# Kernel optimization log

Measured on AMD Instinct MI355X. Metric: run time of the kernel, lower is better.

## Reference

```python
import jax, jax.numpy as jnp
import numpy as np

SEQ, BATCH, IN, HID, OUT = 4096, 64, 64, 256, 1


def setup_inputs() -> dict:
    key = jax.random.key(0)
    ks = jax.random.split(key, 7)
    s = 1.0 / np.sqrt(HID)  # torch GRU/Linear init scale
    return {
        "x": jax.random.normal(ks[0], (SEQ, BATCH, IN), dtype=jnp.float32),
        "w_ih": jax.random.uniform(ks[1], (3 * HID, IN), jnp.float32, -s, s),
        "w_hh": jax.random.uniform(ks[2], (3 * HID, HID), jnp.float32, -s, s),
        "b_ih": jax.random.uniform(ks[3], (3 * HID,), jnp.float32, -s, s),
        "b_hh": jax.random.uniform(ks[4], (3 * HID,), jnp.float32, -s, s),
        "fc_w": jax.random.uniform(ks[5], (OUT, HID), jnp.float32, -s, s),
        "fc_b": jax.random.uniform(ks[6], (OUT,), jnp.float32, -s, s),
    }


def _gru(x, w_ih, w_hh, b_ih, b_hh):
    # x: [S, B, I]. Precompute input-side gate projections in one big GEMM.
    xg = jnp.einsum("sbi,gi->sbg", x, w_ih) + b_ih  # [S, B, 3H]
    H = w_hh.shape[1]
    h0 = jnp.zeros((x.shape[1], H), x.dtype)

    def step(h, xt):
        hg = h @ w_hh.T + b_hh  # [B, 3H]
        xr, xz, xn = jnp.split(xt, 3, axis=-1)
        hr, hz, hn = jnp.split(hg, 3, axis=-1)
        r = jax.nn.sigmoid(xr + hr)
        z = jax.nn.sigmoid(xz + hz)
        n = jnp.tanh(xn + r * hn)  # torch GRU: r gates the hidden-side n term
        h_new = (1.0 - z) * n + z * h
        return h_new, h_new

    _, hs = jax.lax.scan(step, h0, xg)  # hs: [S, B, H]
    return hs


def reference(x, w_ih, w_hh, b_ih, b_hh, fc_w, fc_b):
    hs = _gru(x, w_ih, w_hh, b_ih, b_hh)  # [S, B, H]
    out = hs @ fc_w.T + fc_b  # [S, B, OUT]
    # original does .squeeze(0): no-op since S != 1
    return out
```

## Files before the change

kernel.cpp:

```cpp
#include <hip/hip_runtime.h>

#define SEQ  4096
#define NB   64
#define NI   64
#define NH   256

typedef short  bf16x8 __attribute__((ext_vector_type(8)));
typedef short  bf16x4 __attribute__((ext_vector_type(4)));
typedef float  f32x4  __attribute__((ext_vector_type(4)));

__device__ __forceinline__ unsigned short f2bf(float f) {
    union { float f; unsigned u; } v; v.f = f;
    return (unsigned short)((v.u + 0x7fffu + ((v.u >> 16) & 1u)) >> 16);
}
__device__ __forceinline__ float bflo(int p) {
    union { int i; float f; } u; u.i = p << 16; return u.f;
}
__device__ __forceinline__ float bfhi(int p) {
    union { int i; float f; } u; u.i = p & 0xffff0000; return u.f;
}
__device__ __forceinline__ float fast_rcp(float x) { return __builtin_amdgcn_rcpf(x); }
__device__ __forceinline__ float sigm(float x) { return fast_rcp(1.f + __expf(-x)); }
__device__ __forceinline__ float tanh_(float x) {
    x = fminf(15.f, fmaxf(-15.f, x));
    float e = __expf(2.f * x);
    return (e - 1.f) * fast_rcp(e + 1.f);
}
__device__ __forceinline__ f32x4 mfma16(bf16x8 a, bf16x8 b, f32x4 c) {
    return __builtin_amdgcn_mfma_f32_16x16x32_bf16(a, b, c, 0, 0, 0);
}
__device__ __forceinline__ bf16x8 ldfrag(const float* p) {
    float4 a = *(const float4*)p;
    float4 b = *(const float4*)(p + 4);
    bf16x8 r;
    r[0] = (short)f2bf(a.x); r[1] = (short)f2bf(a.y);
    r[2] = (short)f2bf(a.z); r[3] = (short)f2bf(a.w);
    r[4] = (short)f2bf(b.x); r[5] = (short)f2bf(b.y);
    r[6] = (short)f2bf(b.z); r[7] = (short)f2bf(b.w);
    return r;
}

__global__ __launch_bounds__(1024) void xg_pre(
        const float* __restrict__ x, const float* __restrict__ w_ih,
        const float* __restrict__ b_ih, const float* __restrict__ b_hh,
        short* __restrict__ xg, size_t plane, int t0, int ns)
{
    const int tid = threadIdx.x, wv = tid >> 6, lane = tid & 63;
    const int nn = lane & 15, q = lane >> 4;
    const int jb = wv;

    bf16x8 w[3][2];
    float bias[3];
    #pragma unroll
    for (int g = 0; g < 3; ++g) {
        const int row = g * NH + jb * 16 + nn;
        w[g][0] = ldfrag(w_ih + row * NI + q * 8);
        w[g][1] = ldfrag(w_ih + row * NI + 32 + q * 8);
        bias[g] = b_ih[row] + (g < 2 ? b_hh[row] : 0.f);
    }

    const int NT = ns * 4;
    for (int rt = blockIdx.x; rt < NT; rt += gridDim.x) {
        const float* xr = x + ((size_t)t0 * NB + (size_t)rt * 16 + nn) * NI + q * 8;
        bf16x8 a0 = ldfrag(xr);
        bf16x8 a1 = ldfrag(xr + 32);
        #pragma unroll
        for (int g = 0; g < 3; ++g) {
            f32x4 acc = {0.f, 0.f, 0.f, 0.f};
            acc = mfma16(a0, w[g][0], acc);
            acc = mfma16(a1, w[g][1], acc);
            bf16x4 v;
            #pragma unroll
            for (int m = 0; m < 4; ++m) v[m] = (short)f2bf(acc[m] + bias[g]);
            *(bf16x4*)(xg + (size_t)g * plane +
                       (((size_t)rt * 16 + jb) * 64 + lane) * 4) = v;
        }
    }
}

__global__ __launch_bounds__(1024, 4) void gru_rec(
        const short* __restrict__ xg, size_t plane,
        const float* __restrict__ w_hh,
        const float* __restrict__ b_hh,
        const float* __restrict__ fc_w,
        const float* __restrict__ fc_b,
        float* __restrict__ out,
        float* __restrict__ hcar,
        int t0, int ns)
{
    __shared__ short wlds[65536];
    __shared__ short abuf[8192];
    __shared__ short fcwl[4096];
    __shared__ float oring[1024];

    const int tid = threadIdx.x, wv = tid >> 6, lane = tid & 63;
    const int nn = lane & 15, q = lane >> 4;
    const int bc = blockIdx.x, bbase = bc * 16;

    bf16x8 wr[8], wz[8];
    #pragma unroll
    for (int c = 0; c < 8; ++c)
        wr[c] = ldfrag(w_hh + (0 * NH + wv * 16 + nn) * NH + c * 32 + q * 8);
    #pragma unroll
    for (int c = 0; c < 8; ++c)
        wz[c] = ldfrag(w_hh + (1 * NH + wv * 16 + nn) * NH + c * 32 + q * 8);
    #pragma unroll
    for (int c = 0; c < 8; ++c) {
        bf16x8 f = ldfrag(w_hh + (2 * NH + wv * 16 + nn) * NH + c * 32 + q * 8);
        *(bf16x8*)(wlds + (wv * 8 + c) * 512 + lane * 8) = f;
    }
    if (wv < 8) {
        bf16x8 f = 0;
        if (nn == 0) f = ldfrag(fc_w + wv * 32 + q * 8);
        *(bf16x8*)(fcwl + wv * 512 + lane * 8) = f;
    }
    const float bhn = b_hh[2 * NH + wv * 16 + nn];
    const float fcb = fc_b[0];

    f32x4 hp = {0.f, 0.f, 0.f, 0.f};
    if (t0 == 0) {
        ((int4*)abuf)[tid] = make_int4(0, 0, 0, 0);
    } else {
        #pragma unroll
        for (int m = 0; m < 4; ++m)
            hp[m] = hcar[(size_t)(bbase + q * 4 + m) * NH + wv * 16 + nn];
        const int f = tid * 4, b = f >> 8, k0 = f & 255;
        float4 v = *(const float4*)(hcar + (size_t)(bbase + b) * NH + k0);
        bf16x4 s; s[0] = (short)f2bf(v.x); s[1] = (short)f2bf(v.y);
        s[2] = (short)f2bf(v.z); s[3] = (short)f2bf(v.w);
        *(bf16x4*)(abuf + (k0 >> 5) * 512 + (((k0 >> 3) & 3) * 16 + b) * 8 + (k0 & 7)) = s;
    }

    const int j = wv * 16 + nn;
    const int koff = (j >> 5) * 512 + ((j >> 3) & 3) * 128 + (j & 7) + q * 32;
    const short* xgp = xg + ((size_t)(bc * 16 + wv) * 64 + lane) * 4;
    __syncthreads();

    for (int t = 0; t < ns; ++t) {
        const int cur = t & 1, nxt = cur ^ 1;

        int2 gx = *(const int2*)(xgp);
        int2 gz = *(const int2*)(xgp + plane);
        int2 gn = *(const int2*)(xgp + 2 * plane);
        xgp += 16384;

        if ((t & 31) == 1 && t >= 33 && tid < 512) {
            const int s0 = t - 33;
            out[((size_t)(t0 + s0 + (tid >> 4))) * NB + bbase + (tid & 15)] =
                oring[(((s0 >> 5) & 1) << 9) + (tid >> 4) * 16 + (tid & 15)];
        }

        const bool isfc = (t > 0) && (wv == (t & 15));
        f32x4 ar = {0.f,0.f,0.f,0.f}, az = {0.f,0.f,0.f,0.f};
        f32x4 an = {0.f,0.f,0.f,0.f}, afc = {0.f,0.f,0.f,0.f};
        const short* ab = abuf + cur * 4096;
        #pragma unroll
        for (int c = 0; c < 8; ++c) {
            bf16x8 av = *(const bf16x8*)(ab + c * 512 + lane * 8);
            ar = mfma16(av, wr[c], ar);
            az = mfma16(av, wz[c], az);
            bf16x8 wnf = *(const bf16x8*)(wlds + (wv * 8 + c) * 512 + lane * 8);
            an = mfma16(av, wnf, an);
            if (isfc) {
                bf16x8 ff = *(const bf16x8*)(fcwl + c * 512 + lane * 8);
                afc = mfma16(av, ff, afc);
            }
        }
        if (isfc && nn == 0) {
            const int s = t - 1;
            f32x4 v;
            #pragma unroll
            for (int m = 0; m < 4; ++m) v[m] = afc[m] + fcb;
            *(f32x4*)(oring + (((s >> 5) & 1) << 9) + ((s & 31) << 4) + q * 4) = v;
        }

        const float xr4[4] = { bflo(gx.x), bfhi(gx.x), bflo(gx.y), bfhi(gx.y) };
        const float xz4[4] = { bflo(gz.x), bfhi(gz.x), bflo(gz.y), bfhi(gz.y) };
        const float xn4[4] = { bflo(gn.x), bfhi(gn.x), bflo(gn.y), bfhi(gn.y) };

        short* hw = abuf + nxt * 4096 + koff;
        #pragma unroll
        for (int m = 0; m < 4; ++m) {
            float r_ = sigm(ar[m] + xr4[m]);
            float z_ = sigm(az[m] + xz4[m]);
            float n_ = tanh_(fmaf(r_, an[m] + bhn, xn4[m]));
            float h_ = n_ + z_ * (hp[m] - n_);
            hp[m] = h_;
            hw[m * 8] = (short)f2bf(h_);
        }
        __syncthreads();
    }

    if (wv == 0) {
        const short* ab = abuf + (ns & 1) * 4096;
        f32x4 afc = {0.f, 0.f, 0.f, 0.f};
        #pragma unroll
        for (int c = 0; c < 8; ++c)
            afc = mfma16(*(const bf16x8*)(ab + c * 512 + lane * 8),
                         *(const bf16x8*)(fcwl + c * 512 + lane * 8), afc);
        if (nn == 0) {
            const int s = ns - 1;
            f32x4 v;
            #pragma unroll
            for (int m = 0; m < 4; ++m) v[m] = afc[m] + fcb;
            *(f32x4*)(oring + (((s >> 5) & 1) << 9) + ((s & 31) << 4) + q * 4) = v;
        }
    }
    __syncthreads();
    if (tid < 512) {
        const int s0 = ns - 32;
        out[((size_t)(t0 + s0 + (tid >> 4))) * NB + bbase + (tid & 15)] =
            oring[(((s0 >> 5) & 1) << 9) + (tid >> 4) * 16 + (tid & 15)];
    }
    #pragma unroll
    for (int m = 0; m < 4; ++m)
        hcar[(size_t)(bbase + q * 4 + m) * NH + wv * 16 + nn] = hp[m];
}

extern "C" void kernel_launch(void* const* d_in, const int* in_sizes, int n_in,
                              void* d_out, int out_size, void* d_ws, size_t ws_size,
                              hipStream_t stream) {
    (void)in_sizes; (void)n_in; (void)out_size;
    const float* x    = (const float*)d_in[0];
    const float* w_ih = (const float*)d_in[1];
    const float* w_hh = (const float*)d_in[2];
    const float* b_ih = (const float*)d_in[3];
    const float* b_hh = (const float*)d_in[4];
    const float* fc_w = (const float*)d_in[5];
    const float* fc_b = (const float*)d_in[6];
    float* out  = (float*)d_out;
    float* hcar = (float*)d_ws;
    short* xg   = (short*)((char*)d_ws + 65536);

    const size_t per_step = (size_t)NB * 3 * NH * 2;
    long avail = (long)ws_size - 65536;
    int spc = 64;
    if (avail >= (long)per_step * 64) {
        spc = (int)((avail / (long)per_step) / 64) * 64;
        if (spc > SEQ) spc = SEQ;
    }
    for (int t0 = 0; t0 < SEQ; t0 += spc) {
        int ns = (SEQ - t0 < spc) ? (SEQ - t0) : spc;
        size_t plane = (size_t)spc * 16384;
        xg_pre<<<dim3(2048), dim3(1024), 0, stream>>>(x, w_ih, b_ih, b_hh,
                                                      xg, plane, t0, ns);
        gru_rec<<<dim3(4), dim3(1024), 0, stream>>>(xg, plane, w_hh, b_hh,
                                                    fc_w, fc_b, out, hcar,
                                                    t0, ns);
    }
}
```

Measured before the change: 6.929 ms.

## Fuse input projection and recurrence into one cooperative kernel with producer/consumer overlap

Replaces the per-chunk pair of launches (input-projection GEMM, then 4-block recurrence) with one cooperative kernel of 256 blocks. Four consumer blocks run the GRU recurrence over chunk c while the remaining blocks compute the input-gate projections for chunk c+1 into a double buffer, with a grid sync between chunks. The hidden-state carry through global memory and the serialization of projection behind recurrence go away. In exchange it adds a grid-wide barrier per chunk, depends on all 256 blocks being co-resident, and sizes chunks by workspace (at most 512 steps).

```diff
diff --git a/kernel.cpp b/kernel.cpp
--- a/kernel.cpp
+++ b/kernel.cpp
@@ -1,4 +1,7 @@
 #include <hip/hip_runtime.h>
+#include <hip/hip_cooperative_groups.h>
+
+namespace cg = cooperative_groups;
 
 #define SEQ  4096
 #define NB   64
@@ -40,53 +43,38 @@
     return r;
 }
 
-__global__ __launch_bounds__(1024) void xg_pre(
-        const float* __restrict__ x, const float* __restrict__ w_ih,
-        const float* __restrict__ b_ih, const float* __restrict__ b_hh,
-        short* __restrict__ xg, size_t plane, int t0, int ns)
+__device__ __forceinline__ void prod_tile(
+        const float* __restrict__ x, short* __restrict__ dst, size_t plane,
+        int t0, int rt, int wv, int lane, int nn, int q,
+        const bf16x8 wp[3][2], const float bb[3])
 {
-    const int tid = threadIdx.x, wv = tid >> 6, lane = tid & 63;
-    const int nn = lane & 15, q = lane >> 4;
-    const int jb = wv;
-
-    bf16x8 w[3][2];
-    float bias[3];
+    const float* xr = x + ((size_t)t0 * NB + (size_t)rt * 16 + nn) * NI + q * 8;
+    bf16x8 a0 = ldfrag(xr);
+    bf16x8 a1 = ldfrag(xr + 32);
     #pragma unroll
     for (int g = 0; g < 3; ++g) {
-        const int row = g * NH + jb * 16 + nn;
-        w[g][0] = ldfrag(w_ih + row * NI + q * 8);
-        w[g][1] = ldfrag(w_ih + row * NI + 32 + q * 8);
-        bias[g] = b_ih[row] + (g < 2 ? b_hh[row] : 0.f);
-    }
-
-    const int NT = ns * 4;
-    for (int rt = blockIdx.x; rt < NT; rt += gridDim.x) {
-        const float* xr = x + ((size_t)t0 * NB + (size_t)rt * 16 + nn) * NI + q * 8;
-        bf16x8 a0 = ldfrag(xr);
-        bf16x8 a1 = ldfrag(xr + 32);
-        #pragma unroll
-        for (int g = 0; g < 3; ++g) {
-            f32x4 acc = {0.f, 0.f, 0.f, 0.f};
-            acc = mfma16(a0, w[g][0], acc);
-            acc = mfma16(a1, w[g][1], acc);
-            bf16x4 v;
-            #pragma unroll
-            for (int m = 0; m < 4; ++m) v[m] = (short)f2bf(acc[m] + bias[g]);
-            *(bf16x4*)(xg + (size_t)g * plane +
-                       (((size_t)rt * 16 + jb) * 64 + lane) * 4) = v;
-        }
-    }
-}
-
-__global__ __launch_bounds__(1024, 4) void gru_rec(
-        const short* __restrict__ xg, size_t plane,
+        f32x4 acc = {0.f, 0.f, 0.f, 0.f};
+        acc = mfma16(a0, wp[g][0], acc);
+        acc = mfma16(a1, wp[g][1], acc);
+        bf16x4 v;
+        #pragma unroll
+        for (int m = 0; m < 4; ++m) v[m] = (short)f2bf(acc[m] + bb[g]);
+        *(bf16x4*)(dst + (size_t)g * plane +
+                   (((size_t)rt * 16 + wv) * 64 + lane) * 4) = v;
+    }
+}
+
+__global__ __launch_bounds__(1024, 4) void gru_coop(
+        const float* __restrict__ x,
+        const float* __restrict__ w_ih,
         const float* __restrict__ w_hh,
+        const float* __restrict__ b_ih,
         const float* __restrict__ b_hh,
         const float* __restrict__ fc_w,
         const float* __restrict__ fc_b,
         float* __restrict__ out,
-        float* __restrict__ hcar,
-        int t0, int ns)
+        short* __restrict__ xg,
+        int spc, int nc)
 {
     __shared__ short wlds[65536];
     __shared__ short abuf[8192];
@@ -95,126 +83,149 @@
 
     const int tid = threadIdx.x, wv = tid >> 6, lane = tid & 63;
     const int nn = lane & 15, q = lane >> 4;
-    const int bc = blockIdx.x, bbase = bc * 16;
+    const int bid = blockIdx.x;
+    const bool cons = (bid < 4);
+    const size_t plane = (size_t)spc * 16384;
+    const size_t bufsz = 3 * plane;
+
+    bf16x8 wp[3][2];
+    float bb[3];
+    #pragma unroll
+    for (int g = 0; g < 3; ++g) {
+        const int row = g * NH + wv * 16 + nn;
+        wp[g][0] = ldfrag(w_ih + row * NI + q * 8);
+        wp[g][1] = ldfrag(w_ih + row * NI + 32 + q * 8);
+        bb[g] = b_ih[row] + (g < 2 ? b_hh[row] : 0.f);
+    }
 
     bf16x8 wr[8], wz[8];
-    #pragma unroll
-    for (int c = 0; c < 8; ++c)
-        wr[c] = ldfrag(w_hh + (0 * NH + wv * 16 + nn) * NH + c * 32 + q * 8);
-    #pragma unroll
-    for (int c = 0; c < 8; ++c)
-        wz[c] = ldfrag(w_hh + (1 * NH + wv * 16 + nn) * NH + c * 32 + q * 8);
-    #pragma unroll
-    for (int c = 0; c < 8; ++c) {
-        bf16x8 f = ldfrag(w_hh + (2 * NH + wv * 16 + nn) * NH + c * 32 + q * 8);
-        *(bf16x8*)(wlds + (wv * 8 + c) * 512 + lane * 8) = f;
-    }
-    if (wv < 8) {
-        bf16x8 f = 0;
-        if (nn == 0) f = ldfrag(fc_w + wv * 32 + q * 8);
-        *(bf16x8*)(fcwl + wv * 512 + lane * 8) = f;
-    }
-    const float bhn = b_hh[2 * NH + wv * 16 + nn];
-    const float fcb = fc_b[0];
-
+    float bhn = 0.f, fcb = 0.f;
+    int koff = 0;
+    if (cons) {
+        #pragma unroll
+        for (int c = 0; c < 8; ++c)
+            wr[c] = ldfrag(w_hh + (wv * 16 + nn) * NH + c * 32 + q * 8);
+        #pragma unroll
+        for (int c = 0; c < 8; ++c)
+            wz[c] = ldfrag(w_hh + (NH + wv * 16 + nn) * NH + c * 32 + q * 8);
+        #pragma unroll
+        for (int c = 0; c < 8; ++c) {
+            bf16x8 f = ldfrag(w_hh + (2 * NH + wv * 16 + nn) * NH + c * 32 + q * 8);
+            *(bf16x8*)(wlds + (wv * 8 + c) * 512 + lane * 8) = f;
+        }
+        if (wv < 8) {
+            bf16x8 f = 0;
+            if (nn == 0) f = ldfrag(fc_w + wv * 32 + q * 8);
+            *(bf16x8*)(fcwl + wv * 512 + lane * 8) = f;
+        }
+        bhn = b_hh[2 * NH + wv * 16 + nn];
+        fcb = fc_b[0];
+        ((int4*)abuf)[tid] = make_int4(0, 0, 0, 0);
+        const int j = wv * 16 + nn;
+        koff = (j >> 5) * 512 + ((j >> 3) & 3) * 128 + (j & 7) + q * 32;
+        __syncthreads();
+    }
     f32x4 hp = {0.f, 0.f, 0.f, 0.f};
-    if (t0 == 0) {
-        ((int4*)abuf)[tid] = make_int4(0, 0, 0, 0);
-    } else {
-        #pragma unroll
-        for (int m = 0; m < 4; ++m)
-            hp[m] = hcar[(size_t)(bbase + q * 4 + m) * NH + wv * 16 + nn];
-        const int f = tid * 4, b = f >> 8, k0 = f & 255;
-        float4 v = *(const float4*)(hcar + (size_t)(bbase + b) * NH + k0);
-        bf16x4 s; s[0] = (short)f2bf(v.x); s[1] = (short)f2bf(v.y);
-        s[2] = (short)f2bf(v.z); s[3] = (short)f2bf(v.w);
-        *(bf16x4*)(abuf + (k0 >> 5) * 512 + (((k0 >> 3) & 3) * 16 + b) * 8 + (k0 & 7)) = s;
-    }
-
-    const int j = wv * 16 + nn;
-    const int koff = (j >> 5) * 512 + ((j >> 3) & 3) * 128 + (j & 7) + q * 32;
-    const short* xgp = xg + ((size_t)(bc * 16 + wv) * 64 + lane) * 4;
-    __syncthreads();
-
-    for (int t = 0; t < ns; ++t) {
-        const int cur = t & 1, nxt = cur ^ 1;
-
-        int2 gx = *(const int2*)(xgp);
-        int2 gz = *(const int2*)(xgp + plane);
-        int2 gn = *(const int2*)(xgp + 2 * plane);
-        xgp += 16384;
-
-        if ((t & 31) == 1 && t >= 33 && tid < 512) {
-            const int s0 = t - 33;
-            out[((size_t)(t0 + s0 + (tid >> 4))) * NB + bbase + (tid & 15)] =
+
+    cg::grid_group grid = cg::this_grid();
+
+    {
+        const int NT = spc * 4;
+        for (int rt = bid; rt < NT; rt += gridDim.x)
+            prod_tile(x, xg, plane, 0, rt, wv, lane, nn, q, wp, bb);
+    }
+    grid.sync();
+
+    const int bbase = bid * 16;
+    for (int c = 0; c < nc; ++c) {
+        if (!cons) {
+            if (c + 1 < nc) {
+                short* dst = xg + (size_t)((c + 1) & 1) * bufsz;
+                const int t0 = (c + 1) * spc;
+                const int NT = spc * 4;
+                for (int rt = bid - 4; rt < NT; rt += gridDim.x - 4)
+                    prod_tile(x, dst, plane, t0, rt, wv, lane, nn, q, wp, bb);
+            }
+        } else {
+            const short* xgp = xg + (size_t)(c & 1) * bufsz
+                             + ((size_t)(bid * 16 + wv) * 64 + lane) * 4;
+            for (int tl = 0; tl < spc; ++tl) {
+                const int gt = c * spc + tl;
+
+                int2 gx = *(const int2*)(xgp);
+                int2 gz = *(const int2*)(xgp + plane);
+                int2 gn = *(const int2*)(xgp + 2 * plane);
+                xgp += 16384;
+
+                if ((gt & 31) == 1 && gt >= 33 && tid < 512) {
+                    const int s0 = gt - 33;
+                    out[(size_t)(s0 + (tid >> 4)) * NB + bbase + (tid & 15)] =
+                        oring[(((s0 >> 5) & 1) << 9) + (tid >> 4) * 16 + (tid & 15)];
+                }
+
+                const bool isfc = (gt > 0) && (wv == (gt & 15));
+                f32x4 ar = {0.f,0.f,0.f,0.f}, az = {0.f,0.f,0.f,0.f};
+                f32x4 an = {0.f,0.f,0.f,0.f}, afc = {0.f,0.f,0.f,0.f};
+                const short* ab = abuf + (gt & 1) * 4096;
+                #pragma unroll
+                for (int cc = 0; cc < 8; ++cc) {
+                    bf16x8 av = *(const bf16x8*)(ab + cc * 512 + lane * 8);
+                    ar = mfma16(av, wr[cc], ar);
+                    az = mfma16(av, wz[cc], az);
+                    bf16x8 wnf = *(const bf16x8*)(wlds + (wv * 8 + cc) * 512 + lane * 8);
+                    an = mfma16(av, wnf, an);
+                    if (isfc)
+                        afc = mfma16(av, *(const bf16x8*)(fcwl + cc * 512 + lane * 8), afc);
+                }
+                if (isfc && nn == 0) {
+                    const int s = gt - 1;
+                    f32x4 v;
+                    #pragma unroll
+                    for (int m = 0; m < 4; ++m) v[m] = afc[m] + fcb;
+                    *(f32x4*)(oring + (((s >> 5) & 1) << 9) + ((s & 31) << 4) + q * 4) = v;
+                }
+
+                const float xr4[4] = { bflo(gx.x), bfhi(gx.x), bflo(gx.y), bfhi(gx.y) };
+                const float xz4[4] = { bflo(gz.x), bfhi(gz.x), bflo(gz.y), bfhi(gz.y) };
+                const float xn4[4] = { bflo(gn.x), bfhi(gn.x), bflo(gn.y), bfhi(gn.y) };
+
+                short* hw = abuf + ((gt & 1) ^ 1) * 4096 + koff;
+                #pragma unroll
+                for (int m = 0; m < 4; ++m) {
+                    float r_ = sigm(ar[m] + xr4[m]);
+                    float z_ = sigm(az[m] + xz4[m]);
+                    float n_ = tanh_(fmaf(r_, an[m] + bhn, xn4[m]));
+                    float h_ = n_ + z_ * (hp[m] - n_);
+                    hp[m] = h_;
+                    hw[m * 8] = (short)f2bf(h_);
+                }
+                __syncthreads();
+            }
+        }
+        grid.sync();
+    }
+
+    if (cons) {
+        if (wv == 0) {
+            f32x4 afc = {0.f, 0.f, 0.f, 0.f};
+            #pragma unroll
+            for (int cc = 0; cc < 8; ++cc)
+                afc = mfma16(*(const bf16x8*)(abuf + cc * 512 + lane * 8),
+                             *(const bf16x8*)(fcwl + cc * 512 + lane * 8), afc);
+            if (nn == 0) {
+                const int s = SEQ - 1;
+                #pragma unroll
+                for (int m = 0; m < 4; ++m)
+                    oring[(((s >> 5) & 1) << 9) + ((s & 31) << 4) + q * 4 + m] = afc[m] + fcb;
+            }
+        }
+        __syncthreads();
+        if (tid < 512) {
+            const int s0 = SEQ - 32;
+            out[(size_t)(s0 + (tid >> 4)) * NB + bbase + (tid & 15)] =
                 oring[(((s0 >> 5) & 1) << 9) + (tid >> 4) * 16 + (tid & 15)];
         }
-
-        const bool isfc = (t > 0) && (wv == (t & 15));
-        f32x4 ar = {0.f,0.f,0.f,0.f}, az = {0.f,0.f,0.f,0.f};
-        f32x4 an = {0.f,0.f,0.f,0.f}, afc = {0.f,0.f,0.f,0.f};
-        const short* ab = abuf + cur * 4096;
-        #pragma unroll
-        for (int c = 0; c < 8; ++c) {
-            bf16x8 av = *(const bf16x8*)(ab + c * 512 + lane * 8);
-            ar = mfma16(av, wr[c], ar);
-            az = mfma16(av, wz[c], az);
-            bf16x8 wnf = *(const bf16x8*)(wlds + (wv * 8 + c) * 512 + lane * 8);
-            an = mfma16(av, wnf, an);
-            if (isfc) {
-                bf16x8 ff = *(const bf16x8*)(fcwl + c * 512 + lane * 8);
-                afc = mfma16(av, ff, afc);
-            }
-        }
-        if (isfc && nn == 0) {
-            const int s = t - 1;
-            f32x4 v;
-            #pragma unroll
-            for (int m = 0; m < 4; ++m) v[m] = afc[m] + fcb;
-            *(f32x4*)(oring + (((s >> 5) & 1) << 9) + ((s & 31) << 4) + q * 4) = v;
-        }
-
-        const float xr4[4] = { bflo(gx.x), bfhi(gx.x), bflo(gx.y), bfhi(gx.y) };
-        const float xz4[4] = { bflo(gz.x), bfhi(gz.x), bflo(gz.y), bfhi(gz.y) };
-        const float xn4[4] = { bflo(gn.x), bfhi(gn.x), bflo(gn.y), bfhi(gn.y) };
-
-        short* hw = abuf + nxt * 4096 + koff;
-        #pragma unroll
-        for (int m = 0; m < 4; ++m) {
-            float r_ = sigm(ar[m] + xr4[m]);
-            float z_ = sigm(az[m] + xz4[m]);
-            float n_ = tanh_(fmaf(r_, an[m] + bhn, xn4[m]));
-            float h_ = n_ + z_ * (hp[m] - n_);
-            hp[m] = h_;
-            hw[m * 8] = (short)f2bf(h_);
-        }
-        __syncthreads();
-    }
-
-    if (wv == 0) {
-        const short* ab = abuf + (ns & 1) * 4096;
-        f32x4 afc = {0.f, 0.f, 0.f, 0.f};
-        #pragma unroll
-        for (int c = 0; c < 8; ++c)
-            afc = mfma16(*(const bf16x8*)(ab + c * 512 + lane * 8),
-                         *(const bf16x8*)(fcwl + c * 512 + lane * 8), afc);
-        if (nn == 0) {
-            const int s = ns - 1;
-            f32x4 v;
-            #pragma unroll
-            for (int m = 0; m < 4; ++m) v[m] = afc[m] + fcb;
-            *(f32x4*)(oring + (((s >> 5) & 1) << 9) + ((s & 31) << 4) + q * 4) = v;
-        }
-    }
-    __syncthreads();
-    if (tid < 512) {
-        const int s0 = ns - 32;
-        out[((size_t)(t0 + s0 + (tid >> 4))) * NB + bbase + (tid & 15)] =
-            oring[(((s0 >> 5) & 1) << 9) + (tid >> 4) * 16 + (tid & 15)];
-    }
-    #pragma unroll
-    for (int m = 0; m < 4; ++m)
-        hcar[(size_t)(bbase + q * 4 + m) * NH + wv * 16 + nn] = hp[m];
+    }
 }
 
 extern "C" void kernel_launch(void* const* d_in, const int* in_sizes, int n_in,
@@ -228,24 +239,17 @@
     const float* b_hh = (const float*)d_in[4];
     const float* fc_w = (const float*)d_in[5];
     const float* fc_b = (const float*)d_in[6];
-    float* out  = (float*)d_out;
-    float* hcar = (float*)d_ws;
-    short* xg   = (short*)((char*)d_ws + 65536);
-
-    const size_t per_step = (size_t)NB * 3 * NH * 2;
-    long avail = (long)ws_size - 65536;
+    float* out = (float*)d_out;
+    short* xg  = (short*)d_ws;
+
     int spc = 64;
-    if (avail >= (long)per_step * 64) {
-        spc = (int)((avail / (long)per_step) / 64) * 64;
-        if (spc > SEQ) spc = SEQ;
-    }
-    for (int t0 = 0; t0 < SEQ; t0 += spc) {
-        int ns = (SEQ - t0 < spc) ? (SEQ - t0) : spc;
-        size_t plane = (size_t)spc * 16384;
-        xg_pre<<<dim3(2048), dim3(1024), 0, stream>>>(x, w_ih, b_ih, b_hh,
-                                                      xg, plane, t0, ns);
-        gru_rec<<<dim3(4), dim3(1024), 0, stream>>>(xg, plane, w_hh, b_hh,
-                                                    fc_w, fc_b, out, hcar,
-                                                    t0, ns);
-    }
-}
+    for (int cand = 512; cand >= 64; cand >>= 1)
+        if (2ull * cand * 98304ull <= ws_size) { spc = cand; break; }
+    int nc = SEQ / spc;
+
+    void* args[] = { (void*)&x, (void*)&w_ih, (void*)&w_hh, (void*)&b_ih,
+                     (void*)&b_hh, (void*)&fc_w, (void*)&fc_b, (void*)&out,
+                     (void*)&xg, (void*)&spc, (void*)&nc };
+    hipLaunchCooperativeKernel((const void*)gru_coop, dim3(256), dim3(1024),
+                               args, 0, stream);
+}
```

After: 15.80 ms. +128.0%, slower.
